# Kernel optimization log

Hardware: AMD Instinct MI355X
Metric: run time of the kernel (lower is better)

The kernel has to match this reference:

```python
import jax, jax.numpy as jnp
import numpy as np

N_NODES = 50000


def _graphconv(h, W, b, src, dst, norm_src, norm_dst, activation):
    # DGL GraphConv, norm='both': scale by out-degree^{-1/2} on src side,
    # aggregate (copy_u + sum), scale by in-degree^{-1/2} on dst side.
    in_f, out_f = W.shape
    h = h * norm_src[:, None]
    if in_f > out_f:
        # mult W first to reduce message size (matches DGL branch)
        h = h @ W
        h = jax.ops.segment_sum(h[src], dst, num_segments=N_NODES)
    else:
        h = jax.ops.segment_sum(h[src], dst, num_segments=N_NODES)
        h = h @ W
    h = h * norm_dst[:, None] + b
    if activation:
        h = jax.nn.relu(h)
    return h


def setup_inputs() -> dict:
    key = jax.random.key(0)
    ks = jax.random.split(key, 10)
    N, E = N_NODES, 800000
    in_feats, n_hidden, n_classes = 256, 128, 64
    features = jax.random.normal(ks[0], (N, in_feats), dtype=jnp.float32)
    src = jax.random.randint(ks[1], (E,), 0, N, dtype=jnp.int32)
    dst = jax.random.randint(ks[2], (E,), 0, N, dtype=jnp.int32)
    def glorot(k, shape):
        lim = float(np.sqrt(6.0 / (shape[0] + shape[1])))
        return jax.random.uniform(k, shape, jnp.float32, -lim, lim)
    return {
        "features": features,
        "W1": glorot(ks[3], (in_feats, n_hidden)), "b1": jnp.zeros((n_hidden,), jnp.float32),
        "W2": glorot(ks[4], (n_hidden, n_hidden)), "b2": jnp.zeros((n_hidden,), jnp.float32),
        "W3": glorot(ks[5], (n_hidden, n_classes)), "b3": jnp.zeros((n_classes,), jnp.float32),
        "src": src, "dst": dst,
    }


def reference(features, W1, b1, W2, b2, W3, b3, src, dst):
    ones = jnp.ones(src.shape, jnp.float32)
    deg_out = jax.ops.segment_sum(ones, src, num_segments=N_NODES)
    deg_in = jax.ops.segment_sum(ones, dst, num_segments=N_NODES)
    norm_src = jax.lax.rsqrt(jnp.maximum(deg_out, 1.0))
    norm_dst = jax.lax.rsqrt(jnp.maximum(deg_in, 1.0))
    h = features
    # dropout in eval mode (identity) for deterministic baseline
    h = _graphconv(h, W1, b1, src, dst, norm_src, norm_dst, activation=True)
    h = _graphconv(h, W2, b2, src, dst, norm_src, norm_dst, activation=True)
    h = _graphconv(h, W3, b3, src, dst, norm_src, norm_dst, activation=False)
    return h
```

## Files before the change

### kernel.cpp

```cpp
#include <hip/hip_runtime.h>
#include <math.h>


typedef _Float16 half8 __attribute__((ext_vector_type(8)));
typedef float floatx4 __attribute__((ext_vector_type(4)));

#define TILE 1024
#define BCAP 8192
#define PKW  64
#define EPT  4

__global__ __launch_bounds__(256) void bin_edges(
    const int* __restrict__ src, const int* __restrict__ dst, int E, int NB,
    int* __restrict__ gcurD, int* __restrict__ gcurS,
    ushort2* __restrict__ binD, unsigned short* __restrict__ binS)
{
    __shared__ int lcntD[256], loffD[256], curD[256], lbaseD[256];
    __shared__ int lcntS[256], loffS[256], curS[256], lbaseS[256];
    __shared__ int wtot[4];
    __shared__ ushort2 stageD[TILE];
    __shared__ unsigned short stageS[TILE];

    const int tid = threadIdx.x, lane = tid & 63, wave = tid >> 6;
    const int tile0 = blockIdx.x * TILE;
    const int tn = min(TILE, E - tile0);

    lcntD[tid] = 0;
    lcntS[tid] = 0;
    __syncthreads();

    unsigned short es[EPT], ed[EPT];
    unsigned char ebD[EPT], ebS[EPT];
    int nl = 0;
    for (int i = tid; i < tn; i += 256) {
        int s = src[tile0 + i], d = dst[tile0 + i];
        es[nl] = (unsigned short)s; ed[nl] = (unsigned short)d;
        ebD[nl] = (unsigned char)(d >> 8);
        ebS[nl] = (unsigned char)(s >> 8);
        nl++;
        atomicAdd(&lcntD[d >> 8], 1);
        atomicAdd(&lcntS[s >> 8], 1);
    }
    __syncthreads();

    {
        int v = lcntD[tid], x = v;
#pragma unroll
        for (int o = 1; o < 64; o <<= 1) {
            int t = __shfl_up(x, o, 64);
            if (lane >= o) x += t;
        }
        if (lane == 63) wtot[wave] = x;
        __syncthreads();
        if (tid == 0) {
            int a = 0;
#pragma unroll
            for (int w = 0; w < 4; w++) { int t = wtot[w]; wtot[w] = a; a += t; }
        }
        __syncthreads();
        int excl = x - v + wtot[wave];
        loffD[tid] = excl;
        curD[tid]  = excl;
    }
    __syncthreads();
    {
        int v = lcntS[tid], x = v;
#pragma unroll
        for (int o = 1; o < 64; o <<= 1) {
            int t = __shfl_up(x, o, 64);
            if (lane >= o) x += t;
        }
        if (lane == 63) wtot[wave] = x;
        __syncthreads();
        if (tid == 0) {
            int a = 0;
#pragma unroll
            for (int w = 0; w < 4; w++) { int t = wtot[w]; wtot[w] = a; a += t; }
        }
        __syncthreads();
        int excl = x - v + wtot[wave];
        loffS[tid] = excl;
        curS[tid]  = excl;
    }
    __syncthreads();

    for (int j = 0; j < nl; j++) {
        int pD = atomicAdd(&curD[ebD[j]], 1);
        ushort2 u; u.x = es[j]; u.y = ed[j];
        stageD[pD] = u;
        int pS = atomicAdd(&curS[ebS[j]], 1);
        stageS[pS] = es[j];
    }
    if (tid < NB) {
        if (lcntD[tid] > 0) lbaseD[tid] = atomicAdd(&gcurD[tid], lcntD[tid]);
        if (lcntS[tid] > 0) lbaseS[tid] = atomicAdd(&gcurS[tid], lcntS[tid]);
    }
    __syncthreads();

    for (int i = tid; i < tn; i += 256) {
        {
            int lo = 0, hi = NB - 1;
            while (lo < hi) {
                int mid = (lo + hi + 1) >> 1;
                if (loffD[mid] <= i) lo = mid; else hi = mid - 1;
            }
            int gi = lbaseD[lo] + (i - loffD[lo]);
            if (gi < BCAP)
                binD[(size_t)lo * BCAP + gi] = stageD[i];
        }
        {
            int lo = 0, hi = NB - 1;
            while (lo < hi) {
                int mid = (lo + hi + 1) >> 1;
                if (loffS[mid] <= i) lo = mid; else hi = mid - 1;
            }
            int gi = lbaseS[lo] + (i - loffS[lo]);
            if (gi < BCAP)
                binS[(size_t)lo * BCAP + gi] = stageS[i];
        }
    }
}

__global__ __launch_bounds__(256) void lists_counts(
    const ushort2* __restrict__ binD, const int* __restrict__ gcurD,
    const unsigned short* __restrict__ binS, const int* __restrict__ gcurS,
    unsigned short* __restrict__ packed, int* __restrict__ cntI,
    int* __restrict__ cntO, int N, unsigned short padv)
{
    __shared__ unsigned short stage[256 * PKW];
    __shared__ int lcnt[256];
    __shared__ int h[256];
    const int tid = threadIdx.x;
    const int b = blockIdx.x;
    const int node0 = b << 8;

    lcnt[tid] = 0;
    h[tid] = 0;
    for (int i = tid; i < 256 * PKW; i += 256)
        stage[i] = padv;
    __syncthreads();

    const int nD = min(gcurD[b], BCAP);
    const ushort2* ebD = binD + (size_t)b * BCAP;
    for (int i = tid; i < nD; i += 256) {
        ushort2 e = ebD[i];
        int ld = (int)e.y - node0;
        int p = atomicAdd(&lcnt[ld], 1);
        if (p < PKW) stage[ld * PKW + p] = e.x;
    }
    const int nS = min(gcurS[b], BCAP);
    const unsigned short* ebS = binS + (size_t)b * BCAP;
    for (int i = tid; i < nS; i += 256)
        atomicAdd(&h[(int)ebS[i] - node0], 1);
    __syncthreads();

    int node = node0 + tid;
    if (node < N) {
        cntI[node] = min(lcnt[tid], PKW);
        cntO[node] = h[tid];
    }
    const int wave = tid >> 6, lane = tid & 63;
    for (int ld = wave; ld < 256; ld += 4) {
        int nd = node0 + ld;
        if (nd < N)
            packed[(size_t)nd * PKW + lane] = stage[ld * PKW + lane];
    }
}

__global__ __launch_bounds__(256) void wprep(
    const float* __restrict__ W1, const float* __restrict__ W2,
    const float* __restrict__ W3, _Float16* __restrict__ WT1,
    _Float16* __restrict__ WT2, _Float16* __restrict__ WT3,
    int* __restrict__ gcur, _Float16* __restrict__ z0,
    _Float16* __restrict__ z1)
{
    int i = blockIdx.x * 256 + threadIdx.x;
    if (i < 512) gcur[i] = 0;
    else if (i < 640) z0[i - 512] = (_Float16)0.f;
    else if (i < 768) z1[i - 640] = (_Float16)0.f;
    if (i < 256 * 128) {
        int k = i / 128, n = i - k * 128;
        WT1[(size_t)n * 256 + k] = (_Float16)W1[i];
    } else if (i < 256 * 128 + 128 * 128) {
        int r = i - 256 * 128;
        int k = r / 128, n = r - k * 128;
        WT2[(size_t)n * 128 + k] = (_Float16)W2[r];
    } else if (i < 256 * 128 + 128 * 128 + 128 * 64) {
        int r = i - 256 * 128 - 128 * 128;
        int k = r / 64, n = r - k * 64;
        WT3[(size_t)n * 128 + k] = (_Float16)W3[r];
    }
}

template<int K, int NC, bool A_FP32>
__global__ __launch_bounds__(256) void gemm_mfma(
    const void* __restrict__ A_, const _Float16* __restrict__ WT,
    const int* __restrict__ cnt_rs,
    const int* __restrict__ cnt_nd, const float* __restrict__ bias,
    int do_relu, const int* __restrict__ cnt_ns,
    _Float16* __restrict__ C, int M)
{
    constexpr int NT  = NC / 16;
    constexpr int KC  = 128;
    constexpr int LDW = KC + 8;
    __shared__ _Float16 Bs[NC * LDW];

    const int tid  = threadIdx.x;
    const int wave = tid >> 6;
    const int lane = tid & 63;
    const int quad = lane >> 4;
    const int l16  = lane & 15;

    const int row_base = blockIdx.x * 128 + wave * 32;
    const int ar0 = min(row_base + l16, M - 1);
    const int ar1 = min(row_base + 16 + l16, M - 1);

    floatx4 acc[2][NT];
#pragma unroll
    for (int m = 0; m < 2; m++)
#pragma unroll
        for (int t = 0; t < NT; t++)
            acc[m][t] = (floatx4){0.f, 0.f, 0.f, 0.f};

    float rs0 = 1.0f, rs1 = 1.0f;
    if (A_FP32 && cnt_rs) {
        rs0 = rsqrtf(fmaxf((float)cnt_rs[ar0], 1.0f));
        rs1 = rsqrtf(fmaxf((float)cnt_rs[ar1], 1.0f));
    }

    const float*    Af = (const float*)A_;
    const _Float16* Ah = (const _Float16*)A_;

    for (int kc = 0; kc < K; kc += KC) {
#pragma unroll
        for (int s = tid; s < NC * (KC / 8); s += 256) {
            int row  = s >> 4;
            int col8 = s & 15;
            half8 v = *(const half8*)&WT[(size_t)row * K + kc + col8 * 8];
            *(half8*)&Bs[row * LDW + col8 * 8] = v;
        }
        __syncthreads();
#pragma unroll
        for (int k0 = 0; k0 < KC; k0 += 32) {
            half8 a0, a1;
            if (A_FP32) {
                const float* p0 = &Af[(size_t)ar0 * K + kc + k0 + quad * 8];
                const float* p1 = &Af[(size_t)ar1 * K + kc + k0 + quad * 8];
                float4 f0 = *(const float4*)p0;
                float4 f1 = *(const float4*)(p0 + 4);
                float4 g0 = *(const float4*)p1;
                float4 g1 = *(const float4*)(p1 + 4);
                a0[0] = (_Float16)(f0.x * rs0); a0[1] = (_Float16)(f0.y * rs0);
                a0[2] = (_Float16)(f0.z * rs0); a0[3] = (_Float16)(f0.w * rs0);
                a0[4] = (_Float16)(f1.x * rs0); a0[5] = (_Float16)(f1.y * rs0);
                a0[6] = (_Float16)(f1.z * rs0); a0[7] = (_Float16)(f1.w * rs0);
                a1[0] = (_Float16)(g0.x * rs1); a1[1] = (_Float16)(g0.y * rs1);
                a1[2] = (_Float16)(g0.z * rs1); a1[3] = (_Float16)(g0.w * rs1);
                a1[4] = (_Float16)(g1.x * rs1); a1[5] = (_Float16)(g1.y * rs1);
                a1[6] = (_Float16)(g1.z * rs1); a1[7] = (_Float16)(g1.w * rs1);
            } else {
                a0 = *(const half8*)&Ah[(size_t)ar0 * K + kc + k0 + quad * 8];
                a1 = *(const half8*)&Ah[(size_t)ar1 * K + kc + k0 + quad * 8];
            }
#pragma unroll
            for (int t = 0; t < NT; t++) {
                half8 b = *(const half8*)&Bs[(t * 16 + l16) * LDW + k0 + quad * 8];
                acc[0][t] = __builtin_amdgcn_mfma_f32_16x16x32_f16(a0, b, acc[0][t], 0, 0, 0);
                acc[1][t] = __builtin_amdgcn_mfma_f32_16x16x32_f16(a1, b, acc[1][t], 0, 0, 0);
            }
        }
        __syncthreads();
    }

#pragma unroll
    for (int m = 0; m < 2; m++) {
#pragma unroll
        for (int t = 0; t < NT; t++) {
            int col = t * 16 + l16;
            float bv = bias ? bias[col] : 0.f;
#pragma unroll
            for (int r = 0; r < 4; r++) {
                int row_o = row_base + m * 16 + quad * 4 + r;
                if (row_o < M) {
                    float v = acc[m][t][r];
                    if (cnt_nd) v *= rsqrtf(fmaxf((float)cnt_nd[row_o], 1.0f));
                    v += bv;
                    if (do_relu) v = fmaxf(v, 0.f);
                    if (cnt_ns) v *= rsqrtf(fmaxf((float)cnt_ns[row_o], 1.0f));
                    C[(size_t)row_o * NC + col] = (_Float16)v;
                }
            }
        }
    }
}

__global__ __launch_bounds__(256) void gather128(
    const _Float16* __restrict__ msg, const int* __restrict__ cntI,
    const int* __restrict__ cntO, const unsigned short* __restrict__ packed,
    const float* __restrict__ bias, int do_relu, int use_nd, int use_ns,
    _Float16* __restrict__ out, int N)
{
    int node = (blockIdx.x * 256 + threadIdx.x) >> 6;
    if (node >= N) return;
    int lane = threadIdx.x & 63;
    int grp = lane >> 4, l16 = lane & 15;

    int len = cntI[node];
    const unsigned short* bl = packed + (size_t)node * PKW;
    const half8* mp = (const half8*)msg;

    float a[8];
#pragma unroll
    for (int h = 0; h < 8; h++) a[h] = 0.f;

    int iters = (len + 31) >> 5;
    if (iters < 1) iters = 1;
    for (int it = 0; it < iters; it++) {
        int j = it * 32 + grp;
        int s0 = bl[j],      s1 = bl[j + 4],  s2 = bl[j + 8],  s3 = bl[j + 12];
        int s4 = bl[j + 16], s5 = bl[j + 20], s6 = bl[j + 24], s7 = bl[j + 28];
        half8 v0 = mp[(size_t)s0 * 16 + l16];
        half8 v1 = mp[(size_t)s1 * 16 + l16];
        half8 v2 = mp[(size_t)s2 * 16 + l16];
        half8 v3 = mp[(size_t)s3 * 16 + l16];
        half8 v4 = mp[(size_t)s4 * 16 + l16];
        half8 v5 = mp[(size_t)s5 * 16 + l16];
        half8 v6 = mp[(size_t)s6 * 16 + l16];
        half8 v7 = mp[(size_t)s7 * 16 + l16];
#pragma unroll
        for (int h = 0; h < 8; h++)
            a[h] += (((float)v0[h] + (float)v1[h]) + ((float)v2[h] + (float)v3[h]))
                  + (((float)v4[h] + (float)v5[h]) + ((float)v6[h] + (float)v7[h]));
    }
#pragma unroll
    for (int h = 0; h < 8; h++) {
        a[h] += __shfl_xor(a[h], 16);
        a[h] += __shfl_xor(a[h], 32);
    }

    if (grp == 0) {
        float sc = use_nd ? rsqrtf(fmaxf((float)len, 1.0f)) : 1.0f;
        float pp = use_ns ? rsqrtf(fmaxf((float)cntO[node], 1.0f)) : 1.0f;
        half8 rv;
#pragma unroll
        for (int h = 0; h < 8; h++) {
            float bv = bias ? bias[l16 * 8 + h] : 0.f;
            float r = a[h] * sc + bv;
            if (do_relu) r = fmaxf(r, 0.f);
            rv[h] = (_Float16)(r * pp);
        }
        ((half8*)out)[(size_t)node * 16 + l16] = rv;
    }
}

__global__ __launch_bounds__(256) void gather64(
    const _Float16* __restrict__ msg, const int* __restrict__ cntI,
    const unsigned short* __restrict__ packed, const float* __restrict__ bias,
    float* __restrict__ out, int N)
{
    int node = (blockIdx.x * 256 + threadIdx.x) >> 6;
    if (node >= N) return;
    int lane = threadIdx.x & 63;
    int grp = lane >> 3, l8 = lane & 7;

    int len = cntI[node];
    const unsigned short* bl = packed + (size_t)node * PKW;
    const half8* mp = (const half8*)msg;

    float a[8];
#pragma unroll
    for (int h = 0; h < 8; h++) a[h] = 0.f;

    int iters = (len + 31) >> 5;
    if (iters < 1) iters = 1;
    for (int it = 0; it < iters; it++) {
        int j = it * 32 + grp;
        int s0 = bl[j], s1 = bl[j + 8], s2 = bl[j + 16], s3 = bl[j + 24];
        half8 v0 = mp[(size_t)s0 * 8 + l8];
        half8 v1 = mp[(size_t)s1 * 8 + l8];
        half8 v2 = mp[(size_t)s2 * 8 + l8];
        half8 v3 = mp[(size_t)s3 * 8 + l8];
#pragma unroll
        for (int h = 0; h < 8; h++)
            a[h] += ((float)v0[h] + (float)v1[h]) + ((float)v2[h] + (float)v3[h]);
    }
#pragma unroll
    for (int h = 0; h < 8; h++) {
        a[h] += __shfl_xor(a[h], 8);
        a[h] += __shfl_xor(a[h], 16);
        a[h] += __shfl_xor(a[h], 32);
    }

    if (grp == 0) {
        float sc = rsqrtf(fmaxf((float)len, 1.0f));
        float4 r0, r1;
        r0.x = a[0] * sc + bias[l8 * 8 + 0];
        r0.y = a[1] * sc + bias[l8 * 8 + 1];
        r0.z = a[2] * sc + bias[l8 * 8 + 2];
        r0.w = a[3] * sc + bias[l8 * 8 + 3];
        r1.x = a[4] * sc + bias[l8 * 8 + 4];
        r1.y = a[5] * sc + bias[l8 * 8 + 5];
        r1.z = a[6] * sc + bias[l8 * 8 + 6];
        r1.w = a[7] * sc + bias[l8 * 8 + 7];
        float4* op = (float4*)&out[(size_t)node * 64 + l8 * 8];
        op[0] = r0;
        op[1] = r1;
    }
}

extern "C" void kernel_launch(void* const* d_in, const int* in_sizes, int n_in,
                              void* d_out, int out_size, void* d_ws, size_t ws_size,
                              hipStream_t stream)
{
    const float* X  = (const float*)d_in[0];
    const float* W1 = (const float*)d_in[1];
    const float* b1 = (const float*)d_in[2];
    const float* W2 = (const float*)d_in[3];
    const float* b2 = (const float*)d_in[4];
    const float* W3 = (const float*)d_in[5];
    const float* b3 = (const float*)d_in[6];
    const int*   src = (const int*)d_in[7];
    const int*   dst = (const int*)d_in[8];

    const int N = in_sizes[0] / 256;
    const int E = in_sizes[7];
    const int NB = (N + 255) >> 8;

    char* base = (char*)d_ws;
    size_t cur = 0;
    auto alloc = [&](size_t bytes) -> void* {
        void* p = base + cur;
        cur += (bytes + 255) & ~(size_t)255;
        return p;
    };
    int* gcur2 = (int*)alloc((size_t)2 * 256 * 4);
    int* gcurD = gcur2;
    int* gcurS = gcur2 + 256;
    ushort2*        binD   = (ushort2*)alloc((size_t)NB * BCAP * 4);
    unsigned short* binS   = (unsigned short*)alloc((size_t)NB * BCAP * 2);
    unsigned short* packed = (unsigned short*)alloc((size_t)N * PKW * 2);
    int* cntO = (int*)alloc((size_t)N * 4);
    int* cntI = (int*)alloc((size_t)N * 4);
    _Float16* Bh0 = (_Float16*)alloc(((size_t)N + 1) * 128 * 2);
    _Float16* Bh1 = (_Float16*)alloc(((size_t)N + 1) * 128 * 2);
    _Float16* WT1 = (_Float16*)alloc((size_t)256 * 128 * 2);
    _Float16* WT2 = (_Float16*)alloc((size_t)128 * 128 * 2);
    _Float16* WT3 = (_Float16*)alloc((size_t)128 * 64 * 2);

    const int tblk = (E + TILE - 1) / TILE;
    const int gblk = (N + 127) / 128;
    const int wblk = (N + 3) / 4;

    wprep<<<(256*128 + 128*128 + 128*64 + 255) / 256, 256, 0, stream>>>(
        W1, W2, W3, WT1, WT2, WT3,
        gcur2, Bh0 + (size_t)N * 128, Bh1 + (size_t)N * 128);
    bin_edges<<<tblk, 256, 0, stream>>>(src, dst, E, NB, gcurD, gcurS, binD, binS);
    lists_counts<<<NB, 256, 0, stream>>>(binD, gcurD, binS, gcurS,
                                         packed, cntI, cntO, N,
                                         (unsigned short)N);

    gemm_mfma<256, 128, true><<<gblk, 256, 0, stream>>>(
        X, WT1, cntO, nullptr, nullptr, 0, nullptr, Bh0, N);
    gather128<<<wblk, 256, 0, stream>>>(
        Bh0, cntI, cntO, packed, b1, 1, 1, 1, Bh1, N);

    gather128<<<wblk, 256, 0, stream>>>(
        Bh1, cntI, cntO, packed, nullptr, 0, 0, 0, Bh0, N);
    gemm_mfma<128, 128, false><<<gblk, 256, 0, stream>>>(
        Bh0, WT2, nullptr, cntI, b2, 1, cntO, Bh1, N);

    gemm_mfma<128, 64, false><<<(N + 1 + 127) / 128, 256, 0, stream>>>(
        Bh1, WT3, nullptr, nullptr, nullptr, 0, nullptr, Bh0, N + 1);
    gather64<<<wblk, 256, 0, stream>>>(
        Bh0, cntI, packed, b3, (float*)d_out, N);
}
```

Baseline: 303.6 us.

## Replace two-pass binned CSR build with direct global-atomic adjacency fill

Removes the bin_edges/lists_counts two-kernel bucketing pipeline and its intermediate bin buffers. The prep kernel now pads the packed adjacency and zeroes the degree counters. A new build_graph kernel then uses one global atomic per edge per counter to fill per-node neighbor slots directly. Gather kernels clamp the count to the slot width. This trades shared-memory staging and a kernel launch for scattered global atomics and uncoalesced 2-byte stores, and neighbor order within a node becomes nondeterministic.

```diff
diff --git a/kernel.cpp b/kernel.cpp
--- a/kernel.cpp
+++ b/kernel.cpp
@@ -5,191 +5,52 @@
 typedef _Float16 half8 __attribute__((ext_vector_type(8)));
 typedef float floatx4 __attribute__((ext_vector_type(4)));
 
-#define TILE 1024
-#define BCAP 8192
 #define PKW  64
-#define EPT  4
-
-__global__ __launch_bounds__(256) void bin_edges(
-    const int* __restrict__ src, const int* __restrict__ dst, int E, int NB,
-    int* __restrict__ gcurD, int* __restrict__ gcurS,
-    ushort2* __restrict__ binD, unsigned short* __restrict__ binS)
-{
-    __shared__ int lcntD[256], loffD[256], curD[256], lbaseD[256];
-    __shared__ int lcntS[256], loffS[256], curS[256], lbaseS[256];
-    __shared__ int wtot[4];
-    __shared__ ushort2 stageD[TILE];
-    __shared__ unsigned short stageS[TILE];
-
-    const int tid = threadIdx.x, lane = tid & 63, wave = tid >> 6;
-    const int tile0 = blockIdx.x * TILE;
-    const int tn = min(TILE, E - tile0);
-
-    lcntD[tid] = 0;
-    lcntS[tid] = 0;
-    __syncthreads();
-
-    unsigned short es[EPT], ed[EPT];
-    unsigned char ebD[EPT], ebS[EPT];
-    int nl = 0;
-    for (int i = tid; i < tn; i += 256) {
-        int s = src[tile0 + i], d = dst[tile0 + i];
-        es[nl] = (unsigned short)s; ed[nl] = (unsigned short)d;
-        ebD[nl] = (unsigned char)(d >> 8);
-        ebS[nl] = (unsigned char)(s >> 8);
-        nl++;
-        atomicAdd(&lcntD[d >> 8], 1);
-        atomicAdd(&lcntS[s >> 8], 1);
-    }
-    __syncthreads();
-
-    {
-        int v = lcntD[tid], x = v;
-#pragma unroll
-        for (int o = 1; o < 64; o <<= 1) {
-            int t = __shfl_up(x, o, 64);
-            if (lane >= o) x += t;
-        }
-        if (lane == 63) wtot[wave] = x;
-        __syncthreads();
-        if (tid == 0) {
-            int a = 0;
-#pragma unroll
-            for (int w = 0; w < 4; w++) { int t = wtot[w]; wtot[w] = a; a += t; }
-        }
-        __syncthreads();
-        int excl = x - v + wtot[wave];
-        loffD[tid] = excl;
-        curD[tid]  = excl;
-    }
-    __syncthreads();
-    {
-        int v = lcntS[tid], x = v;
-#pragma unroll
-        for (int o = 1; o < 64; o <<= 1) {
-            int t = __shfl_up(x, o, 64);
-            if (lane >= o) x += t;
-        }
-        if (lane == 63) wtot[wave] = x;
-        __syncthreads();
-        if (tid == 0) {
-            int a = 0;
-#pragma unroll
-            for (int w = 0; w < 4; w++) { int t = wtot[w]; wtot[w] = a; a += t; }
-        }
-        __syncthreads();
-        int excl = x - v + wtot[wave];
-        loffS[tid] = excl;
-        curS[tid]  = excl;
-    }
-    __syncthreads();
-
-    for (int j = 0; j < nl; j++) {
-        int pD = atomicAdd(&curD[ebD[j]], 1);
-        ushort2 u; u.x = es[j]; u.y = ed[j];
-        stageD[pD] = u;
-        int pS = atomicAdd(&curS[ebS[j]], 1);
-        stageS[pS] = es[j];
-    }
-    if (tid < NB) {
-        if (lcntD[tid] > 0) lbaseD[tid] = atomicAdd(&gcurD[tid], lcntD[tid]);
-        if (lcntS[tid] > 0) lbaseS[tid] = atomicAdd(&gcurS[tid], lcntS[tid]);
-    }
-    __syncthreads();
-
-    for (int i = tid; i < tn; i += 256) {
-        {
-            int lo = 0, hi = NB - 1;
-            while (lo < hi) {
-                int mid = (lo + hi + 1) >> 1;
-                if (loffD[mid] <= i) lo = mid; else hi = mid - 1;
-            }
-            int gi = lbaseD[lo] + (i - loffD[lo]);
-            if (gi < BCAP)
-                binD[(size_t)lo * BCAP + gi] = stageD[i];
-        }
-        {
-            int lo = 0, hi = NB - 1;
-            while (lo < hi) {
-                int mid = (lo + hi + 1) >> 1;
-                if (loffS[mid] <= i) lo = mid; else hi = mid - 1;
-            }
-            int gi = lbaseS[lo] + (i - loffS[lo]);
-            if (gi < BCAP)
-                binS[(size_t)lo * BCAP + gi] = stageS[i];
-        }
-    }
-}
-
-__global__ __launch_bounds__(256) void lists_counts(
-    const ushort2* __restrict__ binD, const int* __restrict__ gcurD,
-    const unsigned short* __restrict__ binS, const int* __restrict__ gcurS,
-    unsigned short* __restrict__ packed, int* __restrict__ cntI,
-    int* __restrict__ cntO, int N, unsigned short padv)
-{
-    __shared__ unsigned short stage[256 * PKW];
-    __shared__ int lcnt[256];
-    __shared__ int h[256];
-    const int tid = threadIdx.x;
-    const int b = blockIdx.x;
-    const int node0 = b << 8;
-
-    lcnt[tid] = 0;
-    h[tid] = 0;
-    for (int i = tid; i < 256 * PKW; i += 256)
-        stage[i] = padv;
-    __syncthreads();
-
-    const int nD = min(gcurD[b], BCAP);
-    const ushort2* ebD = binD + (size_t)b * BCAP;
-    for (int i = tid; i < nD; i += 256) {
-        ushort2 e = ebD[i];
-        int ld = (int)e.y - node0;
-        int p = atomicAdd(&lcnt[ld], 1);
-        if (p < PKW) stage[ld * PKW + p] = e.x;
-    }
-    const int nS = min(gcurS[b], BCAP);
-    const unsigned short* ebS = binS + (size_t)b * BCAP;
-    for (int i = tid; i < nS; i += 256)
-        atomicAdd(&h[(int)ebS[i] - node0], 1);
-    __syncthreads();
-
-    int node = node0 + tid;
-    if (node < N) {
-        cntI[node] = min(lcnt[tid], PKW);
-        cntO[node] = h[tid];
-    }
-    const int wave = tid >> 6, lane = tid & 63;
-    for (int ld = wave; ld < 256; ld += 4) {
-        int nd = node0 + ld;
-        if (nd < N)
-            packed[(size_t)nd * PKW + lane] = stage[ld * PKW + lane];
-    }
-}
-
-__global__ __launch_bounds__(256) void wprep(
+
+__global__ __launch_bounds__(256) void prep(
     const float* __restrict__ W1, const float* __restrict__ W2,
     const float* __restrict__ W3, _Float16* __restrict__ WT1,
     _Float16* __restrict__ WT2, _Float16* __restrict__ WT3,
-    int* __restrict__ gcur, _Float16* __restrict__ z0,
-    _Float16* __restrict__ z1)
-{
-    int i = blockIdx.x * 256 + threadIdx.x;
-    if (i < 512) gcur[i] = 0;
-    else if (i < 640) z0[i - 512] = (_Float16)0.f;
-    else if (i < 768) z1[i - 640] = (_Float16)0.f;
+    int* __restrict__ cntI, int* __restrict__ cntO,
+    unsigned short* __restrict__ packed, int N,
+    _Float16* __restrict__ z0, _Float16* __restrict__ z1,
+    unsigned short padv)
+{
+    const int i = blockIdx.x * 256 + threadIdx.x;
+    const int NPK = N * (PKW / 8);
+    if (i < NPK) {
+        unsigned int pp = (unsigned int)padv | ((unsigned int)padv << 16);
+        uint4 v; v.x = pp; v.y = pp; v.z = pp; v.w = pp;
+        ((uint4*)packed)[i] = v;
+    }
+    if (i < N) { cntI[i] = 0; cntO[i] = 0; }
+    if (i < 128) { z0[i] = (_Float16)0.f; z1[i] = (_Float16)0.f; }
     if (i < 256 * 128) {
-        int k = i / 128, n = i - k * 128;
+        int k = i >> 7, n = i & 127;
         WT1[(size_t)n * 256 + k] = (_Float16)W1[i];
-    } else if (i < 256 * 128 + 128 * 128) {
-        int r = i - 256 * 128;
-        int k = r / 128, n = r - k * 128;
-        WT2[(size_t)n * 128 + k] = (_Float16)W2[r];
-    } else if (i < 256 * 128 + 128 * 128 + 128 * 64) {
-        int r = i - 256 * 128 - 128 * 128;
-        int k = r / 64, n = r - k * 64;
-        WT3[(size_t)n * 128 + k] = (_Float16)W3[r];
-    }
+    }
+    if (i < 128 * 128) {
+        int k = i >> 7, n = i & 127;
+        WT2[(size_t)n * 128 + k] = (_Float16)W2[i];
+    }
+    if (i < 128 * 64) {
+        int k = i >> 6, n = i & 63;
+        WT3[(size_t)n * 128 + k] = (_Float16)W3[i];
+    }
+}
+
+__global__ __launch_bounds__(256) void build_graph(
+    const int* __restrict__ src, const int* __restrict__ dst, int E,
+    int* __restrict__ cntI, int* __restrict__ cntO,
+    unsigned short* __restrict__ packed)
+{
+    const int i = blockIdx.x * 256 + threadIdx.x;
+    if (i >= E) return;
+    const int s = src[i], d = dst[i];
+    atomicAdd(&cntO[s], 1);
+    const int p = atomicAdd(&cntI[d], 1);
+    if (p < PKW)
+        packed[(size_t)d * PKW + p] = (unsigned short)s;
 }
 
 template<int K, int NC, bool A_FP32>
@@ -305,7 +166,7 @@
     int lane = threadIdx.x & 63;
     int grp = lane >> 4, l16 = lane & 15;
 
-    int len = cntI[node];
+    int len = min(cntI[node], PKW);
     const unsigned short* bl = packed + (size_t)node * PKW;
     const half8* mp = (const half8*)msg;
 
@@ -363,7 +224,7 @@
     int lane = threadIdx.x & 63;
     int grp = lane >> 3, l8 = lane & 7;
 
-    int len = cntI[node];
+    int len = min(cntI[node], PKW);
     const unsigned short* bl = packed + (size_t)node * PKW;
     const half8* mp = (const half8*)msg;
 
@@ -424,7 +285,6 @@
 
     const int N = in_sizes[0] / 256;
     const int E = in_sizes[7];
-    const int NB = (N + 255) >> 8;
 
     char* base = (char*)d_ws;
     size_t cur = 0;
@@ -433,11 +293,6 @@
         cur += (bytes + 255) & ~(size_t)255;
         return p;
     };
-    int* gcur2 = (int*)alloc((size_t)2 * 256 * 4);
-    int* gcurD = gcur2;
-    int* gcurS = gcur2 + 256;
-    ushort2*        binD   = (ushort2*)alloc((size_t)NB * BCAP * 4);
-    unsigned short* binS   = (unsigned short*)alloc((size_t)NB * BCAP * 2);
     unsigned short* packed = (unsigned short*)alloc((size_t)N * PKW * 2);
     int* cntO = (int*)alloc((size_t)N * 4);
     int* cntI = (int*)alloc((size_t)N * 4);
@@ -447,17 +302,15 @@
     _Float16* WT2 = (_Float16*)alloc((size_t)128 * 128 * 2);
     _Float16* WT3 = (_Float16*)alloc((size_t)128 * 64 * 2);
 
-    const int tblk = (E + TILE - 1) / TILE;
+    const int pblk = (N * (PKW / 8) + 255) / 256;
+    const int bblk = (E + 255) / 256;
     const int gblk = (N + 127) / 128;
     const int wblk = (N + 3) / 4;
 
-    wprep<<<(256*128 + 128*128 + 128*64 + 255) / 256, 256, 0, stream>>>(
-        W1, W2, W3, WT1, WT2, WT3,
-        gcur2, Bh0 + (size_t)N * 128, Bh1 + (size_t)N * 128);
-    bin_edges<<<tblk, 256, 0, stream>>>(src, dst, E, NB, gcurD, gcurS, binD, binS);
-    lists_counts<<<NB, 256, 0, stream>>>(binD, gcurD, binS, gcurS,
-                                         packed, cntI, cntO, N,
-                                         (unsigned short)N);
+    prep<<<pblk, 256, 0, stream>>>(
+        W1, W2, W3, WT1, WT2, WT3, cntI, cntO, packed, N,
+        Bh0 + (size_t)N * 128, Bh1 + (size_t)N * 128, (unsigned short)N);
+    build_graph<<<bblk, 256, 0, stream>>>(src, dst, E, cntI, cntO, packed);
 
     gemm_mfma<256, 128, true><<<gblk, 256, 0, stream>>>(
         X, WT1, cntO, nullptr, nullptr, 0, nullptr, Bh0, N);
```

New measurement: 333.2 us. +9.8%, slower.

## Scatter edges directly to bins, split list build across blocks, shrink gather unroll

Applied to the files above, without the earlier changes.

bin_edges drops the in-LDS stage-and-sort pass (prefix scans, binary-search scatter). Each edge now gets its global slot with a per-bin atomic and is written straight to the bin, with no coalescing. lists_counts is split four ways per bin so each block handles 64 nodes, which raises block count and cuts LDS use. The cost is that every block rescans the whole bin. The gather kernels process 16 neighbours per iteration instead of 32, cutting wasted padded loads for low-degree nodes at the cost of less memory-level parallelism.

```diff
diff --git a/kernel.cpp b/kernel.cpp
--- a/kernel.cpp
+++ b/kernel.cpp
@@ -5,23 +5,21 @@
 typedef _Float16 half8 __attribute__((ext_vector_type(8)));
 typedef float floatx4 __attribute__((ext_vector_type(4)));
 
-#define TILE 1024
-#define BCAP 8192
-#define PKW  64
-#define EPT  4
+#define TILE  1024
+#define BCAP  8192
+#define PKW   64
+#define EPT   4
+#define SPLIT 4
 
 __global__ __launch_bounds__(256) void bin_edges(
     const int* __restrict__ src, const int* __restrict__ dst, int E, int NB,
     int* __restrict__ gcurD, int* __restrict__ gcurS,
     ushort2* __restrict__ binD, unsigned short* __restrict__ binS)
 {
-    __shared__ int lcntD[256], loffD[256], curD[256], lbaseD[256];
-    __shared__ int lcntS[256], loffS[256], curS[256], lbaseS[256];
-    __shared__ int wtot[4];
-    __shared__ ushort2 stageD[TILE];
-    __shared__ unsigned short stageS[TILE];
-
-    const int tid = threadIdx.x, lane = tid & 63, wave = tid >> 6;
+    __shared__ int lcntD[256], curD[256];
+    __shared__ int lcntS[256], curS[256];
+
+    const int tid = threadIdx.x;
     const int tile0 = blockIdx.x * TILE;
     const int tn = min(TILE, E - tile0);
 
@@ -43,81 +41,22 @@
     }
     __syncthreads();
 
-    {
-        int v = lcntD[tid], x = v;
-#pragma unroll
-        for (int o = 1; o < 64; o <<= 1) {
-            int t = __shfl_up(x, o, 64);
-            if (lane >= o) x += t;
-        }
-        if (lane == 63) wtot[wave] = x;
-        __syncthreads();
-        if (tid == 0) {
-            int a = 0;
-#pragma unroll
-            for (int w = 0; w < 4; w++) { int t = wtot[w]; wtot[w] = a; a += t; }
-        }
-        __syncthreads();
-        int excl = x - v + wtot[wave];
-        loffD[tid] = excl;
-        curD[tid]  = excl;
+    if (tid < NB) {
+        curD[tid] = (lcntD[tid] > 0) ? atomicAdd(&gcurD[tid], lcntD[tid]) : 0;
+        curS[tid] = (lcntS[tid] > 0) ? atomicAdd(&gcurS[tid], lcntS[tid]) : 0;
     }
     __syncthreads();
-    {
-        int v = lcntS[tid], x = v;
-#pragma unroll
-        for (int o = 1; o < 64; o <<= 1) {
-            int t = __shfl_up(x, o, 64);
-            if (lane >= o) x += t;
-        }
-        if (lane == 63) wtot[wave] = x;
-        __syncthreads();
-        if (tid == 0) {
-            int a = 0;
-#pragma unroll
-            for (int w = 0; w < 4; w++) { int t = wtot[w]; wtot[w] = a; a += t; }
-        }
-        __syncthreads();
-        int excl = x - v + wtot[wave];
-        loffS[tid] = excl;
-        curS[tid]  = excl;
-    }
-    __syncthreads();
 
     for (int j = 0; j < nl; j++) {
-        int pD = atomicAdd(&curD[ebD[j]], 1);
-        ushort2 u; u.x = es[j]; u.y = ed[j];
-        stageD[pD] = u;
-        int pS = atomicAdd(&curS[ebS[j]], 1);
-        stageS[pS] = es[j];
-    }
-    if (tid < NB) {
-        if (lcntD[tid] > 0) lbaseD[tid] = atomicAdd(&gcurD[tid], lcntD[tid]);
-        if (lcntS[tid] > 0) lbaseS[tid] = atomicAdd(&gcurS[tid], lcntS[tid]);
-    }
-    __syncthreads();
-
-    for (int i = tid; i < tn; i += 256) {
-        {
-            int lo = 0, hi = NB - 1;
-            while (lo < hi) {
-                int mid = (lo + hi + 1) >> 1;
-                if (loffD[mid] <= i) lo = mid; else hi = mid - 1;
-            }
-            int gi = lbaseD[lo] + (i - loffD[lo]);
-            if (gi < BCAP)
-                binD[(size_t)lo * BCAP + gi] = stageD[i];
-        }
-        {
-            int lo = 0, hi = NB - 1;
-            while (lo < hi) {
-                int mid = (lo + hi + 1) >> 1;
-                if (loffS[mid] <= i) lo = mid; else hi = mid - 1;
-            }
-            int gi = lbaseS[lo] + (i - loffS[lo]);
-            if (gi < BCAP)
-                binS[(size_t)lo * BCAP + gi] = stageS[i];
-        }
+        int bD = ebD[j];
+        int pD = atomicAdd(&curD[bD], 1);
+        if (pD < BCAP) {
+            ushort2 u; u.x = es[j]; u.y = ed[j];
+            binD[(size_t)bD * BCAP + pD] = u;
+        }
+        int bS = ebS[j];
+        int pS = atomicAdd(&curS[bS], 1);
+        if (pS < BCAP) binS[(size_t)bS * BCAP + pS] = es[j];
     }
 }
 
@@ -127,41 +66,51 @@
     unsigned short* __restrict__ packed, int* __restrict__ cntI,
     int* __restrict__ cntO, int N, unsigned short padv)
 {
-    __shared__ unsigned short stage[256 * PKW];
-    __shared__ int lcnt[256];
-    __shared__ int h[256];
+    __shared__ unsigned short stage[64 * PKW];
+    __shared__ int lcnt[64];
+    __shared__ int h[64];
     const int tid = threadIdx.x;
-    const int b = blockIdx.x;
-    const int node0 = b << 8;
-
-    lcnt[tid] = 0;
-    h[tid] = 0;
-    for (int i = tid; i < 256 * PKW; i += 256)
-        stage[i] = padv;
+    const int b = blockIdx.x / SPLIT;
+    const int part = blockIdx.x - b * SPLIT;
+    const int nlo = (b << 8) + part * 64;
+
+    if (tid < 64) { lcnt[tid] = 0; h[tid] = 0; }
+    {
+        unsigned int pp = (unsigned int)padv | ((unsigned int)padv << 16);
+        uint4 v; v.x = pp; v.y = pp; v.z = pp; v.w = pp;
+        for (int i = tid; i < 64 * PKW / 8; i += 256)
+            ((uint4*)stage)[i] = v;
+    }
     __syncthreads();
 
     const int nD = min(gcurD[b], BCAP);
     const ushort2* ebD = binD + (size_t)b * BCAP;
     for (int i = tid; i < nD; i += 256) {
         ushort2 e = ebD[i];
-        int ld = (int)e.y - node0;
-        int p = atomicAdd(&lcnt[ld], 1);
-        if (p < PKW) stage[ld * PKW + p] = e.x;
+        int ld = (int)e.y - nlo;
+        if ((unsigned)ld < 64u) {
+            int p = atomicAdd(&lcnt[ld], 1);
+            if (p < PKW) stage[ld * PKW + p] = e.x;
+        }
     }
     const int nS = min(gcurS[b], BCAP);
     const unsigned short* ebS = binS + (size_t)b * BCAP;
-    for (int i = tid; i < nS; i += 256)
-        atomicAdd(&h[(int)ebS[i] - node0], 1);
+    for (int i = tid; i < nS; i += 256) {
+        int ls = (int)ebS[i] - nlo;
+        if ((unsigned)ls < 64u) atomicAdd(&h[ls], 1);
+    }
     __syncthreads();
 
-    int node = node0 + tid;
-    if (node < N) {
-        cntI[node] = min(lcnt[tid], PKW);
-        cntO[node] = h[tid];
+    if (tid < 64) {
+        int node = nlo + tid;
+        if (node < N) {
+            cntI[node] = min(lcnt[tid], PKW);
+            cntO[node] = h[tid];
+        }
     }
     const int wave = tid >> 6, lane = tid & 63;
-    for (int ld = wave; ld < 256; ld += 4) {
-        int nd = node0 + ld;
+    for (int ld = wave; ld < 64; ld += 4) {
+        int nd = nlo + ld;
         if (nd < N)
             packed[(size_t)nd * PKW + lane] = stage[ld * PKW + lane];
     }
@@ -305,7 +254,7 @@
     int lane = threadIdx.x & 63;
     int grp = lane >> 4, l16 = lane & 15;
 
-    int len = cntI[node];
+    int len = min(cntI[node], PKW);
     const unsigned short* bl = packed + (size_t)node * PKW;
     const half8* mp = (const half8*)msg;
 
@@ -313,24 +262,18 @@
 #pragma unroll
     for (int h = 0; h < 8; h++) a[h] = 0.f;
 
-    int iters = (len + 31) >> 5;
+    int iters = (len + 15) >> 4;
     if (iters < 1) iters = 1;
     for (int it = 0; it < iters; it++) {
-        int j = it * 32 + grp;
-        int s0 = bl[j],      s1 = bl[j + 4],  s2 = bl[j + 8],  s3 = bl[j + 12];
-        int s4 = bl[j + 16], s5 = bl[j + 20], s6 = bl[j + 24], s7 = bl[j + 28];
+        int j = it * 16 + grp;
+        int s0 = bl[j], s1 = bl[j + 4], s2 = bl[j + 8], s3 = bl[j + 12];
         half8 v0 = mp[(size_t)s0 * 16 + l16];
         half8 v1 = mp[(size_t)s1 * 16 + l16];
         half8 v2 = mp[(size_t)s2 * 16 + l16];
         half8 v3 = mp[(size_t)s3 * 16 + l16];
-        half8 v4 = mp[(size_t)s4 * 16 + l16];
-        half8 v5 = mp[(size_t)s5 * 16 + l16];
-        half8 v6 = mp[(size_t)s6 * 16 + l16];
-        half8 v7 = mp[(size_t)s7 * 16 + l16];
 #pragma unroll
         for (int h = 0; h < 8; h++)
-            a[h] += (((float)v0[h] + (float)v1[h]) + ((float)v2[h] + (float)v3[h]))
-                  + (((float)v4[h] + (float)v5[h]) + ((float)v6[h] + (float)v7[h]));
+            a[h] += ((float)v0[h] + (float)v1[h]) + ((float)v2[h] + (float)v3[h]);
     }
 #pragma unroll
     for (int h = 0; h < 8; h++) {
@@ -363,7 +306,7 @@
     int lane = threadIdx.x & 63;
     int grp = lane >> 3, l8 = lane & 7;
 
-    int len = cntI[node];
+    int len = min(cntI[node], PKW);
     const unsigned short* bl = packed + (size_t)node * PKW;
     const half8* mp = (const half8*)msg;
 
@@ -371,18 +314,16 @@
 #pragma unroll
     for (int h = 0; h < 8; h++) a[h] = 0.f;
 
-    int iters = (len + 31) >> 5;
+    int iters = (len + 15) >> 4;
     if (iters < 1) iters = 1;
     for (int it = 0; it < iters; it++) {
-        int j = it * 32 + grp;
-        int s0 = bl[j], s1 = bl[j + 8], s2 = bl[j + 16], s3 = bl[j + 24];
+        int j = it * 16 + grp;
+        int s0 = bl[j], s1 = bl[j + 8];
         half8 v0 = mp[(size_t)s0 * 8 + l8];
         half8 v1 = mp[(size_t)s1 * 8 + l8];
-        half8 v2 = mp[(size_t)s2 * 8 + l8];
-        half8 v3 = mp[(size_t)s3 * 8 + l8];
 #pragma unroll
         for (int h = 0; h < 8; h++)
-            a[h] += ((float)v0[h] + (float)v1[h]) + ((float)v2[h] + (float)v3[h]);
+            a[h] += (float)v0[h] + (float)v1[h];
     }
 #pragma unroll
     for (int h = 0; h < 8; h++) {
@@ -455,9 +396,9 @@
         W1, W2, W3, WT1, WT2, WT3,
         gcur2, Bh0 + (size_t)N * 128, Bh1 + (size_t)N * 128);
     bin_edges<<<tblk, 256, 0, stream>>>(src, dst, E, NB, gcurD, gcurS, binD, binS);
-    lists_counts<<<NB, 256, 0, stream>>>(binD, gcurD, binS, gcurS,
-                                         packed, cntI, cntO, N,
-                                         (unsigned short)N);
+    lists_counts<<<NB * SPLIT, 256, 0, stream>>>(binD, gcurD, binS, gcurS,
+                                                 packed, cntI, cntO, N,
+                                                 (unsigned short)N);
 
     gemm_mfma<256, 128, true><<<gblk, 256, 0, stream>>>(
         X, WT1, cntO, nullptr, nullptr, 0, nullptr, Bh0, N);
```

After: 297.5 us. 1.02x faster.
